# Performance work log

Measured on AMD Instinct MI355X. Metric: run time of the kernel, lower is better.

The kernel has to match this reference:

```python
import jax, jax.numpy as jnp
import numpy as np
import math

B, T, D, H = 1, 2048, 1024, 16
DH = D // H  # 64


def relative_shift(x):
    # x: [B, H, T, S] -> Transformer-XL relative shift via zero-pad + reshape
    b, h, t, s = x.shape
    zero_pad = jnp.zeros((b, h, t, 1), dtype=x.dtype)
    x_padded = jnp.concatenate([zero_pad, x], axis=-1)       # [B,H,T,S+1]
    x_padded = x_padded.reshape(b, h, s + 1, t)              # [B,H,S+1,T]
    return x_padded[:, :, 1:].reshape(b, h, t, s)            # [B,H,T,S]


def setup_inputs() -> dict:
    key = jax.random.key(0)
    ks = jax.random.split(key, 9)
    std = 0.02
    return {
        "x": jax.random.normal(ks[0], (B, T, D), dtype=jnp.float32),
        "r_emb": jax.random.normal(ks[1], (T, D), dtype=jnp.float32),
        "Wq": jax.random.normal(ks[2], (D, D), dtype=jnp.float32) * std,
        "Wk": jax.random.normal(ks[3], (D, D), dtype=jnp.float32) * std,
        "Wv": jax.random.normal(ks[4], (D, D), dtype=jnp.float32) * std,
        "Wr": jax.random.normal(ks[5], (D, D), dtype=jnp.float32) * std,
        "Wo": jax.random.normal(ks[6], (D, D), dtype=jnp.float32) * std,
        "u": jax.random.normal(ks[7], (H, DH), dtype=jnp.float32) * std,
        "v_bias": jax.random.normal(ks[8], (H, DH), dtype=jnp.float32) * std,
    }


def reference(x, r_emb, Wq, Wk, Wv, Wr, Wo, u, v_bias):
    # mem=None path (the only shape-consistent path in the source), so S == T.
    b, t, d = x.shape
    s = t
    q = (x @ Wq).reshape(b, t, H, DH).transpose(0, 2, 1, 3)   # [B,H,T,DH]
    k = (x @ Wk).reshape(b, s, H, DH).transpose(0, 2, 1, 3)   # [B,H,S,DH]
    v = (x @ Wv).reshape(b, s, H, DH).transpose(0, 2, 1, 3)   # [B,H,S,DH]
    r = (r_emb @ Wr).reshape(r_emb.shape[0], H, DH)[-s:]       # [S,H,DH]

    AC = jnp.einsum('bhid,bhjd->bhij', q + u[None, :, None, :], k)
    BD = jnp.einsum('bhid,jhd->bhij', q + v_bias[None, :, None, :], r)
    BD = relative_shift(BD)

    attn = (AC + BD) / math.sqrt(DH)                           # [B,H,T,S]
    mask = jnp.tril(jnp.ones((t, s), dtype=bool))              # causal (S==T)
    attn = jnp.where(mask[None, None], attn, -jnp.inf)
    attn = jax.nn.softmax(attn, axis=-1)
    # dropout is identity in eval mode
    out = jnp.einsum('bhij,bhjd->bhid', attn, v)               # [B,H,T,DH]
    out = out.transpose(0, 2, 1, 3).reshape(b, t, d)           # [B,T,D]
    return out @ Wo
```

## Files before the change

### kernel.cpp

```cpp
#include <hip/hip_runtime.h>

typedef __bf16 bf16_t;
typedef __bf16 bf16x4v __attribute__((ext_vector_type(4)));
typedef __bf16 bf16x8 __attribute__((ext_vector_type(8)));
typedef float f32x4 __attribute__((ext_vector_type(4)));

constexpr int TT = 2048;
constexpr int DDIM = 1024;

constexpr size_t SZ_TD  = (size_t)2048 * 1024;
constexpr size_t OFF_QU = 0;
constexpr size_t OFF_QV = 1 * SZ_TD;
constexpr size_t OFF_KK = 2 * SZ_TD;
constexpr size_t OFF_RR = 3 * SZ_TD;
constexpr size_t OFF_VT = 4 * SZ_TD;
constexpr size_t OFF_AO = 5 * SZ_TD;
constexpr size_t OFF_XB = 6 * SZ_TD;
constexpr size_t OFF_RB = 7 * SZ_TD;
constexpr size_t OFF_WT = 8 * SZ_TD;
constexpr size_t SZ_W   = (size_t)1024 * 1024;

__device__ __forceinline__ f32x4 fzero4() {
  f32x4 z; z[0] = 0.f; z[1] = 0.f; z[2] = 0.f; z[3] = 0.f; return z;
}

__device__ __forceinline__ void gload16(const bf16_t* g, bf16_t* l) {
  __builtin_amdgcn_global_load_lds((const __attribute__((address_space(1))) void*)g,
                                   (__attribute__((address_space(3))) void*)l, 16, 0, 0);
}

__global__ __launch_bounds__(256) void convert_kernel(const float* __restrict__ x,
                                                      const float* __restrict__ r,
                                                      bf16_t* __restrict__ ws) {
  const int i = blockIdx.x * 256 + threadIdx.x;
  float4 a = ((const float4*)x)[i];
  float4 b = ((const float4*)r)[i];
  bf16x4v av, bv;
  av[0] = (bf16_t)a.x; av[1] = (bf16_t)a.y; av[2] = (bf16_t)a.z; av[3] = (bf16_t)a.w;
  bv[0] = (bf16_t)b.x; bv[1] = (bf16_t)b.y; bv[2] = (bf16_t)b.z; bv[3] = (bf16_t)b.w;
  ((bf16x4v*)(ws + OFF_XB))[i] = av;
  ((bf16x4v*)(ws + OFF_RB))[i] = bv;
}

__global__ __launch_bounds__(256) void transpose_w_kernel(const float* __restrict__ Wq,
                                                          const float* __restrict__ Wk,
                                                          const float* __restrict__ Wv,
                                                          const float* __restrict__ Wr,
                                                          const float* __restrict__ Wo,
                                                          bf16_t* __restrict__ ws) {
  const int k0 = blockIdx.x * 64, n0 = blockIdx.y * 64, wsel = blockIdx.z;
  const float* W = (wsel == 0) ? Wq : (wsel == 1) ? Wk : (wsel == 2) ? Wv : (wsel == 3) ? Wr : Wo;
  bf16_t* Wt = ws + OFF_WT + (size_t)wsel * SZ_W;
  __shared__ float tile[64][65];
  const int tid = threadIdx.x;
#pragma unroll
  for (int it = 0; it < 4; ++it) {
    int g = tid + it * 256; int rr = g >> 4; int c4 = (g & 15) * 4;
    float4 v = *(const float4*)&W[(size_t)(k0 + rr) * DDIM + n0 + c4];
    tile[rr][c4] = v.x; tile[rr][c4 + 1] = v.y; tile[rr][c4 + 2] = v.z; tile[rr][c4 + 3] = v.w;
  }
  __syncthreads();
#pragma unroll
  for (int it = 0; it < 4; ++it) {
    int g = tid + it * 256; int nr = g >> 4; int c4 = (g & 15) * 4;
    bf16x4v o;
    o[0] = (bf16_t)tile[c4 + 0][nr]; o[1] = (bf16_t)tile[c4 + 1][nr];
    o[2] = (bf16_t)tile[c4 + 2][nr]; o[3] = (bf16_t)tile[c4 + 3][nr];
    *(bf16x4v*)&Wt[(size_t)(n0 + nr) * DDIM + k0 + c4] = o;
  }
}

__device__ __forceinline__ void gemm128_core(const bf16_t* __restrict__ A,
                                             const bf16_t* __restrict__ Bt,
                                             int i0, int n0, int kbeg, int kend,
                                             f32x4 acc[4][4],
                                             bf16_t* As, bf16_t* Bs) {
  const int tid = threadIdx.x, lane = tid & 63, wv = tid >> 6;
  const int wr = (wv >> 1) * 64, wc = (wv & 1) * 64;
  const int sr = tid >> 2, scc = (tid & 3) * 8;
  const int l15 = lane & 15, lg8 = (lane >> 4) * 8;
  for (int k0 = kbeg; k0 < kend; k0 += 32) {
    __syncthreads();
    gload16(&A[(size_t)(i0 + sr) * DDIM + k0 + scc],       &As[sr * 32 + scc]);
    gload16(&A[(size_t)(i0 + 64 + sr) * DDIM + k0 + scc],  &As[(64 + sr) * 32 + scc]);
    gload16(&Bt[(size_t)(n0 + sr) * DDIM + k0 + scc],      &Bs[sr * 32 + scc]);
    gload16(&Bt[(size_t)(n0 + 64 + sr) * DDIM + k0 + scc], &Bs[(64 + sr) * 32 + scc]);
    __syncthreads();
    bf16x8 af[4], bfv[4];
#pragma unroll
    for (int m = 0; m < 4; ++m) af[m] = *(const bf16x8*)&As[(wr + m * 16 + l15) * 32 + lg8];
#pragma unroll
    for (int n = 0; n < 4; ++n) bfv[n] = *(const bf16x8*)&Bs[(wc + n * 16 + l15) * 32 + lg8];
#pragma unroll
    for (int m = 0; m < 4; ++m)
#pragma unroll
      for (int n = 0; n < 4; ++n)
        acc[m][n] = __builtin_amdgcn_mfma_f32_16x16x32_bf16(af[m], bfv[n], acc[m][n], 0, 0, 0);
  }
}

__global__ __launch_bounds__(256) void proj_kernel(const bf16_t* wsc, bf16_t* wsd,
                                                   const float* __restrict__ u,
                                                   const float* __restrict__ vb) {
  const int z = blockIdx.z;
  const int i0 = blockIdx.x * 128, n0 = blockIdx.y * 128;
  const bf16_t* A = wsc + ((z == 3) ? OFF_RB : OFF_XB);
  const bf16_t* Bt = wsc + OFF_WT + (size_t)z * SZ_W;
  __shared__ bf16_t As[128 * 32];
  __shared__ bf16_t Bs[128 * 32];
  const int lane = threadIdx.x & 63, wv = threadIdx.x >> 6;
  const int wr = (wv >> 1) * 64, wc = (wv & 1) * 64;
  const int l15 = lane & 15, lr4 = (lane >> 4) * 4;
  f32x4 acc[4][4];
#pragma unroll
  for (int m = 0; m < 4; ++m)
#pragma unroll
    for (int n = 0; n < 4; ++n) acc[m][n] = fzero4();

  gemm128_core(A, Bt, i0, n0, 0, DDIM, acc, As, Bs);

#pragma unroll
  for (int mm = 0; mm < 4; ++mm)
#pragma unroll
    for (int nn = 0; nn < 4; ++nn)
#pragma unroll
      for (int rg = 0; rg < 4; ++rg) {
        const int row = i0 + wr + mm * 16 + lr4 + rg;
        const int col = n0 + wc + nn * 16 + l15;
        const float val = acc[mm][nn][rg];
        const int hh = col >> 6, dh = col & 63;
        if (z == 0) {
          wsd[OFF_QU + ((size_t)hh * TT + row) * 64 + dh] = (bf16_t)(val + u[col]);
          wsd[OFF_QV + ((size_t)hh * TT + row) * 64 + dh] = (bf16_t)(val + vb[col]);
        } else if (z == 1) {
          wsd[OFF_KK + ((size_t)hh * TT + row) * 64 + dh] = (bf16_t)val;
        } else if (z == 2) {
          wsd[OFF_VT + ((size_t)hh * 64 + dh) * TT + row] = (bf16_t)val;
        } else {
          wsd[OFF_RR + ((size_t)hh * TT + (TT - 1 - row)) * 64 + dh] = (bf16_t)val;
        }
      }
}

#define LOADK(DST, JJ)                                                                     \
  _Pragma("unroll") for (int nt_ = 0; nt_ < 4; ++nt_)                                      \
  _Pragma("unroll") for (int ks_ = 0; ks_ < 2; ++ks_)                                      \
    DST[nt_][ks_] = *(const bf16x8*)&Kp[(size_t)((JJ) + nt_ * 16 + l15) * 64 + ks_ * 32 + lg8];

#define ATTN_BODY(KC, KN, J0, JN)                                                          \
  {                                                                                        \
    bf16x8 rf[5][2];                                                                       \
    const int c0 = iw0 - (J0) - 63;                                                        \
    _Pragma("unroll") for (int bt = 0; bt < 5; ++bt) {                                     \
      int c = c0 + bt * 16 + l15;                                                          \
      c = (c < 0) ? 0 : ((c > TT - 1) ? TT - 1 : c);                                       \
      _Pragma("unroll") for (int ks = 0; ks < 2; ++ks)                                     \
        rf[bt][ks] = *(const bf16x8*)&Rp[(size_t)c * 64 + ks * 32 + lg8];                  \
    }                                                                                      \
    bf16x8 vf[4][2];                                                                       \
    _Pragma("unroll") for (int d = 0; d < 4; ++d)                                          \
      _Pragma("unroll") for (int ks = 0; ks < 2; ++ks)                                     \
        vf[d][ks] = *(const bf16x8*)&Vp[(size_t)(d * 16 + l15) * TT + (J0) + ks * 32 + lg8];\
    LOADK(KN, JN)                                                                          \
    f32x4 ac[4];                                                                           \
    _Pragma("unroll") for (int nt = 0; nt < 4; ++nt) ac[nt] = fzero4();                    \
    _Pragma("unroll") for (int nt = 0; nt < 4; ++nt)                                       \
      _Pragma("unroll") for (int ks = 0; ks < 2; ++ks)                                     \
        ac[nt] = __builtin_amdgcn_mfma_f32_16x16x32_bf16(KC[nt][ks], qu[ks], ac[nt], 0, 0, 0); \
    f32x4 bd[5];                                                                           \
    _Pragma("unroll") for (int bt = 0; bt < 5; ++bt) bd[bt] = fzero4();                    \
    _Pragma("unroll") for (int bt = 0; bt < 5; ++bt)                                       \
      _Pragma("unroll") for (int ks = 0; ks < 2; ++ks)                                     \
        bd[bt] = __builtin_amdgcn_mfma_f32_16x16x32_bf16(rf[bt][ks], qv[ks], bd[bt], 0, 0, 0); \
    _Pragma("unroll") for (int bt = 0; bt < 5; ++bt)                                       \
      _Pragma("unroll") for (int rg = 0; rg < 4; ++rg)                                     \
        PB[(bt * 16 + lg * 4 + rg) * 17 + l15] = bd[bt][rg];                               \
    float sc[4][4];                                                                        \
    float smax = -3e38f;                                                                   \
    _Pragma("unroll") for (int nt = 0; nt < 4; ++nt)                                       \
      _Pragma("unroll") for (int rg = 0; rg < 4; ++rg) {                                   \
        const int jj = nt * 16 + lg * 4 + rg;                                              \
        float v = (ac[nt][rg] + PB[(l15 + 63 - jj) * 17 + l15]) * 0.125f;                  \
        v = ((J0) + jj > iw0 + l15) ? -1e30f : v;                                          \
        smax = fmaxf(smax, v);                                                             \
        sc[nt][rg] = v;                                                                    \
      }                                                                                    \
    smax = fmaxf(smax, __shfl_xor(smax, 16));                                              \
    smax = fmaxf(smax, __shfl_xor(smax, 32));                                              \
    const float newm = fmaxf(mrun, smax);                                                  \
    const float fac = __expf(mrun - newm);                                                 \
    mrun = newm;                                                                           \
    float pv[4][4];                                                                        \
    float rsum = 0.f;                                                                      \
    _Pragma("unroll") for (int nt = 0; nt < 4; ++nt)                                       \
      _Pragma("unroll") for (int rg = 0; rg < 4; ++rg) {                                   \
        pv[nt][rg] = __expf(sc[nt][rg] - newm);                                            \
        rsum += pv[nt][rg];                                                                \
      }                                                                                    \
    rsum += __shfl_xor(rsum, 16);                                                          \
    rsum += __shfl_xor(rsum, 32);                                                          \
    lrun = lrun * fac + rsum;                                                              \
    float fo[4];                                                                           \
    _Pragma("unroll") for (int rg = 0; rg < 4; ++rg) fo[rg] = __shfl(fac, lg * 4 + rg);    \
    _Pragma("unroll") for (int d = 0; d < 4; ++d)                                          \
      _Pragma("unroll") for (int rg = 0; rg < 4; ++rg) o[d][rg] *= fo[rg];                 \
    _Pragma("unroll") for (int nt = 0; nt < 4; ++nt) {                                     \
      bf16x4v pk;                                                                          \
      pk[0] = (bf16_t)pv[nt][0]; pk[1] = (bf16_t)pv[nt][1];                                \
      pk[2] = (bf16_t)pv[nt][2]; pk[3] = (bf16_t)pv[nt][3];                                \
      *(bf16x4v*)&PL[l15 * 72 + nt * 16 + lg * 4] = pk;                                    \
    }                                                                                      \
    bf16x8 pf[2];                                                                          \
    _Pragma("unroll") for (int ks = 0; ks < 2; ++ks)                                       \
      pf[ks] = *(const bf16x8*)&PL[l15 * 72 + ks * 32 + lg8];                              \
    _Pragma("unroll") for (int d = 0; d < 4; ++d)                                          \
      _Pragma("unroll") for (int ks = 0; ks < 2; ++ks)                                     \
        o[d] = __builtin_amdgcn_mfma_f32_16x16x32_bf16(pf[ks], vf[d][ks], o[d], 0, 0, 0);  \
  }

__global__ __launch_bounds__(128) void attn_kernel(const bf16_t* wsc, bf16_t* wsd) {
  const int h = blockIdx.x;
  const int chunk = blockIdx.z;
  const int q32 = 63 - blockIdx.y;
  const int i0 = q32 * 32;
  const int tid = threadIdx.x;
  const int lane = tid & 63;
  const int wv = tid >> 6;
  const int iw0 = i0 + wv * 16;
  const int l15 = lane & 15;
  const int lg = lane >> 4;
  const int lg8 = lg * 8;

  const int NT = (i0 >> 6) + 1;
  const int H = (NT + 1) >> 1;
  const int tbeg = chunk ? H : 0;
  const int tend = chunk ? NT : H;

  bf16_t* Po = wsd + OFF_XB + (size_t)(chunk * 16 + h) * TT * 64;
  float2* ml = (float2*)(wsd + OFF_WT) + (size_t)(chunk * 16 + h) * TT;

  if (tbeg >= tend) {
#pragma unroll
    for (int d = 0; d < 4; ++d)
#pragma unroll
      for (int rg = 0; rg < 4; ++rg)
        Po[(size_t)(iw0 + lg * 4 + rg) * 64 + d * 16 + l15] = (bf16_t)0.f;
    if (lg == 0) ml[iw0 + l15] = make_float2(-3e38f, 0.f);
    return;
  }

  const bf16_t* QUp = wsc + OFF_QU + (size_t)h * TT * 64;
  const bf16_t* QVp = wsc + OFF_QV + (size_t)h * TT * 64;
  const bf16_t* Kp  = wsc + OFF_KK + (size_t)h * TT * 64;
  const bf16_t* Rp  = wsc + OFF_RR + (size_t)h * TT * 64;
  const bf16_t* Vp  = wsc + OFF_VT + (size_t)h * 64 * TT;

  __shared__ float PbandS[2][80 * 17];
  __shared__ bf16_t PldsS[2][16 * 72];
  float* PB = PbandS[wv];
  bf16_t* PL = PldsS[wv];

  bf16x8 qu[2], qv[2];
#pragma unroll
  for (int ks = 0; ks < 2; ++ks) {
    qu[ks] = *(const bf16x8*)&QUp[(size_t)(iw0 + l15) * 64 + ks * 32 + lg8];
    qv[ks] = *(const bf16x8*)&QVp[(size_t)(iw0 + l15) * 64 + ks * 32 + lg8];
  }

  f32x4 o[4];
#pragma unroll
  for (int d = 0; d < 4; ++d) o[d] = fzero4();
  float mrun = -3e38f, lrun = 0.f;

  bf16x8 kA[4][2], kB[4][2];
  LOADK(kA, tbeg * 64)

  int t = tbeg;
  while (true) {
    int j0 = t * 64;
    int tn = (t + 1 < tend) ? t + 1 : t;
    ATTN_BODY(kA, kB, j0, tn * 64)
    if (++t >= tend) break;
    j0 = t * 64;
    tn = (t + 1 < tend) ? t + 1 : t;
    ATTN_BODY(kB, kA, j0, tn * 64)
    if (++t >= tend) break;
  }

#pragma unroll
  for (int d = 0; d < 4; ++d)
#pragma unroll
    for (int rg = 0; rg < 4; ++rg)
      Po[(size_t)(iw0 + lg * 4 + rg) * 64 + d * 16 + l15] = (bf16_t)o[d][rg];
  if (lg == 0) ml[iw0 + l15] = make_float2(mrun, lrun);
}

__global__ __launch_bounds__(256) void combine_kernel(const bf16_t* wsc, bf16_t* wsd) {
  const int gid = blockIdx.x * 256 + threadIdx.x;
  const int row = gid >> 3;
  const int colg = (gid & 7) * 8;
  const float2* mlp = (const float2*)(wsc + OFF_WT);
  const float2 ml0 = mlp[row];
  const float2 ml1 = mlp[16 * TT + row];
  const float M = fmaxf(ml0.x, ml1.x);
  const float e0 = __expf(ml0.x - M), e1 = __expf(ml1.x - M);
  const float inv = 1.f / (ml0.y * e0 + ml1.y * e1);
  bf16x8 o0 = *(const bf16x8*)&wsc[OFF_XB + (size_t)row * 64 + colg];
  bf16x8 o1 = *(const bf16x8*)&wsc[OFF_XB + ((size_t)16 * TT + row) * 64 + colg];
  const int hh = row >> 11, tt2 = row & 2047;
  bf16x8 r;
#pragma unroll
  for (int i = 0; i < 8; ++i)
    r[i] = (bf16_t)(((float)o0[i] * e0 + (float)o1[i] * e1) * inv);
  *(bf16x8*)&wsd[OFF_AO + (size_t)tt2 * DDIM + hh * 64 + colg] = r;
}

__global__ __launch_bounds__(256) void outproj_kernel(const bf16_t* wsc, float* __restrict__ outp) {
  const int i0 = blockIdx.x * 128, n0 = blockIdx.y * 128, kz = blockIdx.z;
  const bf16_t* A = wsc + OFF_AO;
  const bf16_t* Bt = wsc + OFF_WT + 4 * SZ_W;
  __shared__ bf16_t As[128 * 32];
  __shared__ bf16_t Bs[128 * 32];
  const int lane = threadIdx.x & 63, wv = threadIdx.x >> 6;
  const int wr = (wv >> 1) * 64, wc = (wv & 1) * 64;
  const int l15 = lane & 15, lr4 = (lane >> 4) * 4;
  f32x4 acc[4][4];
#pragma unroll
  for (int m = 0; m < 4; ++m)
#pragma unroll
    for (int n = 0; n < 4; ++n) acc[m][n] = fzero4();

  gemm128_core(A, Bt, i0, n0, kz * 256, kz * 256 + 256, acc, As, Bs);

#pragma unroll
  for (int mm = 0; mm < 4; ++mm)
#pragma unroll
    for (int nn = 0; nn < 4; ++nn)
#pragma unroll
      for (int rg = 0; rg < 4; ++rg) {
        const int row = i0 + wr + mm * 16 + lr4 + rg;
        const int col = n0 + wc + nn * 16 + l15;
        atomicAdd(&outp[(size_t)row * DDIM + col], acc[mm][nn][rg]);
      }
}

extern "C" void kernel_launch(void* const* d_in, const int* in_sizes, int n_in,
                              void* d_out, int out_size, void* d_ws, size_t ws_size,
                              hipStream_t stream) {
  (void)in_sizes; (void)n_in; (void)out_size; (void)ws_size;
  const float* x    = (const float*)d_in[0];
  const float* remb = (const float*)d_in[1];
  const float* Wq   = (const float*)d_in[2];
  const float* Wk   = (const float*)d_in[3];
  const float* Wv   = (const float*)d_in[4];
  const float* Wr   = (const float*)d_in[5];
  const float* Wo   = (const float*)d_in[6];
  const float* u    = (const float*)d_in[7];
  const float* vb   = (const float*)d_in[8];
  bf16_t* ws = (bf16_t*)d_ws;
  float* outp = (float*)d_out;

  hipMemsetAsync(outp, 0, (size_t)TT * DDIM * sizeof(float), stream);
  convert_kernel<<<dim3(2048), 256, 0, stream>>>(x, remb, ws);
  transpose_w_kernel<<<dim3(16, 16, 5), 256, 0, stream>>>(Wq, Wk, Wv, Wr, Wo, ws);
  proj_kernel<<<dim3(16, 8, 4), 256, 0, stream>>>(ws, ws, u, vb);
  attn_kernel<<<dim3(16, 64, 2), 128, 0, stream>>>(ws, ws);
  combine_kernel<<<dim3(1024), 256, 0, stream>>>(ws, ws);
  outproj_kernel<<<dim3(16, 8, 4), 256, 0, stream>>>(ws, outp);
}
```

Baseline: 278.1 us.

## Split attention into three KV chunks with single-wave blocks; narrow projection tiles

The attention kernel now runs one 64-thread wave per 16-row query block and splits the causal key range three ways instead of two. The partial outputs go to separate workspace regions, and combine merges three (max, sum) partials. The projection GEMM uses 128x64 tiles with its own inline loop, doubling the grid. The goal is more parallelism and better load balance across CUs, at the cost of more partial-output traffic, a heavier combine, and less reuse per projection tile.

Result: no change. 276.5 us (-0.6%).

```diff
diff --git a/kernel.cpp b/kernel.cpp
--- a/kernel.cpp
+++ b/kernel.cpp
@@ -19,6 +19,7 @@
 constexpr size_t OFF_RB = 7 * SZ_TD;
 constexpr size_t OFF_WT = 8 * SZ_TD;
 constexpr size_t SZ_W   = (size_t)1024 * 1024;
+constexpr size_t OFF_P2 = OFF_WT + SZ_W;
 
 __device__ __forceinline__ f32x4 fzero4() {
   f32x4 z; z[0] = 0.f; z[1] = 0.f; z[2] = 0.f; z[3] = 0.f; return z;
@@ -103,26 +104,43 @@
                                                    const float* __restrict__ u,
                                                    const float* __restrict__ vb) {
   const int z = blockIdx.z;
-  const int i0 = blockIdx.x * 128, n0 = blockIdx.y * 128;
+  const int i0 = blockIdx.x * 128, n0 = blockIdx.y * 64;
   const bf16_t* A = wsc + ((z == 3) ? OFF_RB : OFF_XB);
   const bf16_t* Bt = wsc + OFF_WT + (size_t)z * SZ_W;
   __shared__ bf16_t As[128 * 32];
-  __shared__ bf16_t Bs[128 * 32];
-  const int lane = threadIdx.x & 63, wv = threadIdx.x >> 6;
-  const int wr = (wv >> 1) * 64, wc = (wv & 1) * 64;
-  const int l15 = lane & 15, lr4 = (lane >> 4) * 4;
-  f32x4 acc[4][4];
+  __shared__ bf16_t Bs[64 * 32];
+  const int tid = threadIdx.x, lane = tid & 63, wv = tid >> 6;
+  const int wr = (wv >> 1) * 64, wc = (wv & 1) * 32;
+  const int sr = tid >> 2, scc = (tid & 3) * 8;
+  const int l15 = lane & 15, lg8 = (lane >> 4) * 8, lr4 = (lane >> 4) * 4;
+  f32x4 acc[4][2];
 #pragma unroll
   for (int m = 0; m < 4; ++m)
 #pragma unroll
-    for (int n = 0; n < 4; ++n) acc[m][n] = fzero4();
-
-  gemm128_core(A, Bt, i0, n0, 0, DDIM, acc, As, Bs);
+    for (int n = 0; n < 2; ++n) acc[m][n] = fzero4();
+
+  for (int k0 = 0; k0 < DDIM; k0 += 32) {
+    __syncthreads();
+    gload16(&A[(size_t)(i0 + sr) * DDIM + k0 + scc],      &As[sr * 32 + scc]);
+    gload16(&A[(size_t)(i0 + 64 + sr) * DDIM + k0 + scc], &As[(64 + sr) * 32 + scc]);
+    gload16(&Bt[(size_t)(n0 + sr) * DDIM + k0 + scc],     &Bs[sr * 32 + scc]);
+    __syncthreads();
+    bf16x8 af[4], bfv[2];
+#pragma unroll
+    for (int m = 0; m < 4; ++m) af[m] = *(const bf16x8*)&As[(wr + m * 16 + l15) * 32 + lg8];
+#pragma unroll
+    for (int n = 0; n < 2; ++n) bfv[n] = *(const bf16x8*)&Bs[(wc + n * 16 + l15) * 32 + lg8];
+#pragma unroll
+    for (int m = 0; m < 4; ++m)
+#pragma unroll
+      for (int n = 0; n < 2; ++n)
+        acc[m][n] = __builtin_amdgcn_mfma_f32_16x16x32_bf16(af[m], bfv[n], acc[m][n], 0, 0, 0);
+  }
 
 #pragma unroll
   for (int mm = 0; mm < 4; ++mm)
 #pragma unroll
-    for (int nn = 0; nn < 4; ++nn)
+    for (int nn = 0; nn < 2; ++nn)
 #pragma unroll
       for (int rg = 0; rg < 4; ++rg) {
         const int row = i0 + wr + mm * 16 + lr4 + rg;
@@ -218,25 +236,23 @@
         o[d] = __builtin_amdgcn_mfma_f32_16x16x32_bf16(pf[ks], vf[d][ks], o[d], 0, 0, 0);  \
   }
 
-__global__ __launch_bounds__(128) void attn_kernel(const bf16_t* wsc, bf16_t* wsd) {
+__global__ __launch_bounds__(64) void attn_kernel(const bf16_t* wsc, bf16_t* wsd) {
   const int h = blockIdx.x;
   const int chunk = blockIdx.z;
-  const int q32 = 63 - blockIdx.y;
-  const int i0 = q32 * 32;
-  const int tid = threadIdx.x;
-  const int lane = tid & 63;
-  const int wv = tid >> 6;
-  const int iw0 = i0 + wv * 16;
+  const int q16 = 127 - blockIdx.y;
+  const int iw0 = q16 * 16;
+  const int lane = threadIdx.x & 63;
   const int l15 = lane & 15;
   const int lg = lane >> 4;
   const int lg8 = lg * 8;
 
-  const int NT = (i0 >> 6) + 1;
-  const int H = (NT + 1) >> 1;
-  const int tbeg = chunk ? H : 0;
-  const int tend = chunk ? NT : H;
-
-  bf16_t* Po = wsd + OFF_XB + (size_t)(chunk * 16 + h) * TT * 64;
+  const int NT = (q16 >> 2) + 1;
+  const int base = NT / 3, rem = NT % 3;
+  const int tbeg = chunk * base + (chunk < rem ? chunk : rem);
+  const int tend = tbeg + base + (chunk < rem ? 1 : 0);
+
+  bf16_t* Po = wsd + ((chunk == 0) ? OFF_XB : (chunk == 1) ? OFF_RB : OFF_P2)
+             + (size_t)h * TT * 64;
   float2* ml = (float2*)(wsd + OFF_WT) + (size_t)(chunk * 16 + h) * TT;
 
   if (tbeg >= tend) {
@@ -255,10 +271,8 @@
   const bf16_t* Rp  = wsc + OFF_RR + (size_t)h * TT * 64;
   const bf16_t* Vp  = wsc + OFF_VT + (size_t)h * 64 * TT;
 
-  __shared__ float PbandS[2][80 * 17];
-  __shared__ bf16_t PldsS[2][16 * 72];
-  float* PB = PbandS[wv];
-  bf16_t* PL = PldsS[wv];
+  __shared__ float PB[80 * 17];
+  __shared__ bf16_t PL[16 * 72];
 
   bf16x8 qu[2], qv[2];
 #pragma unroll
@@ -302,16 +316,18 @@
   const float2* mlp = (const float2*)(wsc + OFF_WT);
   const float2 ml0 = mlp[row];
   const float2 ml1 = mlp[16 * TT + row];
-  const float M = fmaxf(ml0.x, ml1.x);
-  const float e0 = __expf(ml0.x - M), e1 = __expf(ml1.x - M);
-  const float inv = 1.f / (ml0.y * e0 + ml1.y * e1);
+  const float2 ml2 = mlp[32 * TT + row];
+  const float M = fmaxf(fmaxf(ml0.x, ml1.x), ml2.x);
+  const float e0 = __expf(ml0.x - M), e1 = __expf(ml1.x - M), e2 = __expf(ml2.x - M);
+  const float inv = 1.f / (ml0.y * e0 + ml1.y * e1 + ml2.y * e2);
   bf16x8 o0 = *(const bf16x8*)&wsc[OFF_XB + (size_t)row * 64 + colg];
-  bf16x8 o1 = *(const bf16x8*)&wsc[OFF_XB + ((size_t)16 * TT + row) * 64 + colg];
+  bf16x8 o1 = *(const bf16x8*)&wsc[OFF_RB + (size_t)row * 64 + colg];
+  bf16x8 o2 = *(const bf16x8*)&wsc[OFF_P2 + (size_t)row * 64 + colg];
   const int hh = row >> 11, tt2 = row & 2047;
   bf16x8 r;
 #pragma unroll
   for (int i = 0; i < 8; ++i)
-    r[i] = (bf16_t)(((float)o0[i] * e0 + (float)o1[i] * e1) * inv);
+    r[i] = (bf16_t)(((float)o0[i] * e0 + (float)o1[i] * e1 + (float)o2[i] * e2) * inv);
   *(bf16x8*)&wsd[OFF_AO + (size_t)tt2 * DDIM + hh * 64 + colg] = r;
 }
 
@@ -363,8 +379,8 @@
   hipMemsetAsync(outp, 0, (size_t)TT * DDIM * sizeof(float), stream);
   convert_kernel<<<dim3(2048), 256, 0, stream>>>(x, remb, ws);
   transpose_w_kernel<<<dim3(16, 16, 5), 256, 0, stream>>>(Wq, Wk, Wv, Wr, Wo, ws);
-  proj_kernel<<<dim3(16, 8, 4), 256, 0, stream>>>(ws, ws, u, vb);
-  attn_kernel<<<dim3(16, 64, 2), 128, 0, stream>>>(ws, ws);
+  proj_kernel<<<dim3(16, 16, 4), 256, 0, stream>>>(ws, ws, u, vb);
+  attn_kernel<<<dim3(16, 128, 3), 64, 0, stream>>>(ws, ws);
   combine_kernel<<<dim3(1024), 256, 0, stream>>>(ws, ws);
   outproj_kernel<<<dim3(16, 8, 4), 256, 0, stream>>>(ws, outp);
 }
```
